# Kernel tuning notes

Hardware: AMD Instinct MI355X
Metric: run time of the kernel (lower is better)

The kernel has to match this reference:

```python
import jax, jax.numpy as jnp
import numpy as np

LN_EPS = 1e-5
NEG_SLOPE = 0.2
INF = float((1 << 32) - 1)


def _ln(x, g, b):
    m = x.mean(-1, keepdims=True)
    v = ((x - m) ** 2).mean(-1, keepdims=True)
    return (x - m) * jax.lax.rsqrt(v + LN_EPS) * g + b


def setup_inputs() -> dict:
    B, M, NPG = 128, 256, 192      # graphs, max nodes per graph, actual nodes per graph
    N = B * NPG                    # 24576 total nodes
    E = N * 16                     # 393216 edges (avg degree 16)
    d, H, Od = 256, 4, 64          # input/attn dim, heads, per-head dim
    out_dim = 256
    key = jax.random.key(0)
    ks = jax.random.split(key, 24)
    s = 0.05
    p = lambda k, sh: jax.random.normal(k, sh, jnp.float32) * s

    node_feat = jax.random.normal(ks[0], (N, d), jnp.float32)
    edge_feat = jax.random.normal(ks[1], (E, d), jnp.float32)
    edge_index = jax.random.randint(ks[2], (2, E), 0, N)
    ptr = jnp.arange(B + 1, dtype=jnp.int32) * NPG
    row_valid = jnp.arange(M) < NPG
    attn_mask = jnp.broadcast_to(row_valid[None, :, None] & row_valid[None, None, :], (B, M, M))

    return dict(
        node_feat=node_feat, attn_mask=attn_mask, edge_feat=edge_feat,
        edge_index=edge_index, num_nodes=N, ptr=ptr,
        Wq=p(ks[3], (d, H * Od)), Wk=p(ks[4], (d, H * Od)), Wv=p(ks[5], (d, H * Od)),
        alphaQ=p(ks[6], (H, Od)), alphaK=p(ks[7], (H, Od)), attn_bias=p(ks[8], (H, Od)),
        gin_eps=jnp.zeros((), jnp.float32),
        gin_W1=p(ks[9], (d, 2 * d)), gin_b1=jnp.zeros((2 * d,), jnp.float32),
        gin_W2=p(ks[10], (2 * d, d)), gin_b2=jnp.zeros((d,), jnp.float32),
        ln1_g=jnp.ones((d,), jnp.float32), ln1_b=jnp.zeros((d,), jnp.float32),
        ln2_g=jnp.ones((d,), jnp.float32), ln2_b=jnp.zeros((d,), jnp.float32),
        ff_W1=p(ks[11], (2 * d, out_dim)), ff_b1=jnp.zeros((out_dim,), jnp.float32),
        ff_W2=p(ks[12], (out_dim, out_dim)), ff_b2=jnp.zeros((out_dim,), jnp.float32),
    )


def reference(node_feat, attn_mask, edge_feat, edge_index, num_nodes, ptr,
              Wq, Wk, Wv, alphaQ, alphaK, attn_bias,
              gin_eps, gin_W1, gin_b1, gin_W2, gin_b2,
              ln1_g, ln1_b, ln2_g, ln2_b,
              ff_W1, ff_b1, ff_W2, ff_b2):
    B, M = attn_mask.shape[:2]
    N, d = node_feat.shape
    H = alphaQ.shape[0]

    # graph -> dense batch layout (scatter by (graph, local position))
    node_ids = jnp.arange(N)
    batch_id = jnp.searchsorted(ptr, node_ids, side='right') - 1
    local = node_ids - ptr[batch_id]
    attn_input = jnp.zeros((B, M, d), node_feat.dtype).at[batch_id, local].set(node_feat)

    # GAT-style additive multi-head attention
    Qp = (attn_input @ Wq).reshape(B, M, H, -1)
    Kp = (attn_input @ Wk).reshape(B, M, H, -1)
    Vp = (attn_input @ Wv).reshape(B, M, H, -1)
    aQ = jnp.einsum('bmhd,hd->bmh', Qp, alphaQ)
    aK = jnp.einsum('bmhd,hd->bmh', Kp, alphaK)
    w = jax.nn.leaky_relu(aQ[:, :, None, :] + aK[:, None, :, :], NEG_SLOPE)  # [B,Q,K,H]
    w = jnp.where(attn_mask[..., None], w, -INF)
    w = jax.nn.softmax(w, axis=2)
    attn_out = (jnp.einsum('bqkh,bkhd->bqhd', w, Vp) + attn_bias).reshape(B, M, -1)

    attn_res = _ln(attn_out + attn_input, ln1_g, ln1_b)[batch_id, local]  # back to [N, d]

    # GIN conv: relu(x[dst] + e) scatter-summed to src, then 2-layer MLP
    msg = jax.nn.relu(node_feat[edge_index[1]] + edge_feat)
    agg = jax.ops.segment_sum(msg, edge_index[0], num_segments=num_nodes)
    h = (1.0 + gin_eps) * node_feat + agg
    gin = jax.nn.relu(h @ gin_W1 + gin_b1) @ gin_W2 + gin_b2
    gin_res = _ln(gin + node_feat, ln2_g, ln2_b)

    x = jnp.concatenate([gin_res, attn_res], axis=-1)  # [N, 2d]
    return jax.nn.relu(x @ ff_W1 + ff_b1) @ ff_W2 + ff_b2
```

## Files before the change

### kernel.cpp

```cpp
#include <hip/hip_runtime.h>

#define LN_EPS 1e-5f
#define NEG_SLOPE 0.2f

typedef __attribute__((ext_vector_type(8))) short short8;
typedef __attribute__((ext_vector_type(4))) float f32x4;

__device__ __forceinline__ unsigned short f2bf(float f) {
  union { float f; unsigned int u; } v;
  v.f = f;
  unsigned int r = v.u + 0x7fffu + ((v.u >> 16) & 1u);
  return (unsigned short)(r >> 16);
}
__device__ __forceinline__ float bf2f(unsigned short u) {
  union { unsigned int u; float f; } v;
  v.u = ((unsigned int)u) << 16;
  return v.f;
}

__global__ __launch_bounds__(256) void k_fold(
    const float* __restrict__ Wq, const float* __restrict__ Wk,
    const float* __restrict__ alphaQ, const float* __restrict__ alphaK,
    float* __restrict__ wqa, float* __restrict__ wka) {
  int t = threadIdx.x;
  for (int h = 0; h < 4; ++h) {
    float sq = 0.f, sk = 0.f;
    for (int od = 0; od < 64; ++od) {
      sq += Wq[t * 256 + h * 64 + od] * alphaQ[h * 64 + od];
      sk += Wk[t * 256 + h * 64 + od] * alphaK[h * 64 + od];
    }
    wqa[t * 4 + h] = sq;
    wka[t * 4 + h] = sk;
  }
}

__global__ __launch_bounds__(256) void k_mega(
    const float* __restrict__ Wv, const float* __restrict__ gW1,
    const float* __restrict__ gW2, const float* __restrict__ fW1,
    const float* __restrict__ fW2, unsigned short* __restrict__ wvt,
    unsigned short* __restrict__ w1t, unsigned short* __restrict__ w2t,
    unsigned short* __restrict__ fw1t, unsigned short* __restrict__ fw2t,
    int* __restrict__ ideg, int Nn, const float* __restrict__ node_feat,
    unsigned short* __restrict__ nf16, const float* __restrict__ wqa,
    const float* __restrict__ wka, float* __restrict__ aQ,
    float* __restrict__ aK) {
  const int bid = blockIdx.x;
  if (bid < 2048) {
    int i = bid * 256 + threadIdx.x;
    const float* src;
    unsigned short* dst;
    int K, N, base;
    if (i < 65536) {
      src = Wv; dst = wvt; K = 256; N = 256; base = 0;
    } else if (i < 196608) {
      src = gW1; dst = w1t; K = 256; N = 512; base = 65536;
    } else if (i < 327680) {
      src = gW2; dst = w2t; K = 512; N = 256; base = 196608;
    } else if (i < 458752) {
      src = fW1; dst = fw1t; K = 512; N = 256; base = 327680;
    } else {
      src = fW2; dst = fw2t; K = 256; N = 256; base = 458752;
    }
    int j = i - base;
    int n = j / K, k = j - n * K;
    dst[j] = f2bf(src[(size_t)k * N + n]);
    return;
  }
  if (bid < 2144) {
    int i = (bid - 2048) * 256 + threadIdx.x;
    if (i < Nn) ideg[i] = 0;
    return;
  }
  const int n = (bid - 2144) * 4 + (threadIdx.x >> 6);
  const int lane = threadIdx.x & 63;
  f32x4 x = ((const f32x4*)node_feat)[(size_t)n * 64 + lane];
  ushort4 o;
  o.x = f2bf(x.x);
  o.y = f2bf(x.y);
  o.z = f2bf(x.z);
  o.w = f2bf(x.w);
  ((ushort4*)nf16)[(size_t)n * 64 + lane] = o;
  float sq[4], sk[4];
  const int d0 = lane * 4;
#pragma unroll
  for (int h = 0; h < 4; ++h) {
    sq[h] = x.x * wqa[(d0 + 0) * 4 + h] + x.y * wqa[(d0 + 1) * 4 + h] +
            x.z * wqa[(d0 + 2) * 4 + h] + x.w * wqa[(d0 + 3) * 4 + h];
    sk[h] = x.x * wka[(d0 + 0) * 4 + h] + x.y * wka[(d0 + 1) * 4 + h] +
            x.z * wka[(d0 + 2) * 4 + h] + x.w * wka[(d0 + 3) * 4 + h];
  }
#pragma unroll
  for (int off = 32; off; off >>= 1) {
#pragma unroll
    for (int h = 0; h < 4; ++h) {
      sq[h] += __shfl_xor(sq[h], off);
      sk[h] += __shfl_xor(sk[h], off);
    }
  }
  if (lane == 0) {
#pragma unroll
    for (int h = 0; h < 4; ++h) {
      aQ[(size_t)n * 4 + h] = sq[h];
      aK[(size_t)n * 4 + h] = sk[h];
    }
  }
}

template <bool RELU, bool BIAS, bool OUTBF>
__global__ __launch_bounds__(256) void k_gemm16(
    const unsigned short* __restrict__ A, const unsigned short* __restrict__ Bt,
    const float* __restrict__ bias, void* __restrict__ Cv, int M, int N,
    int K) {
  __shared__ uint4 As[512];
  __shared__ uint4 Bs[1024];
  const int tid = threadIdx.x;
  const int wid = tid >> 6;
  const int lane = tid & 63;
  const int row0 = blockIdx.x * 64;
  const int col0 = blockIdx.y * 128;
  const int wr = wid >> 1;
  const int wc = wid & 1;
  const int fr = lane & 15;
  const int fq = lane >> 4;

  f32x4 acc[2][4];
#pragma unroll
  for (int m = 0; m < 2; ++m)
#pragma unroll
    for (int n = 0; n < 4; ++n) acc[m][n] = (f32x4){0.f, 0.f, 0.f, 0.f};

  for (int k0 = 0; k0 < K; k0 += 64) {
    __syncthreads();
#pragma unroll
    for (int c = 0; c < 2; ++c) {
      int idx = c * 256 + tid;
      int row = idx >> 3, slot = idx & 7;
      As[row * 8 + (slot ^ (row & 7))] =
          *(const uint4*)(A + (size_t)(row0 + row) * K + k0 + slot * 8);
    }
#pragma unroll
    for (int c = 0; c < 4; ++c) {
      int idx = c * 256 + tid;
      int row = idx >> 3, slot = idx & 7;
      Bs[row * 8 + (slot ^ (row & 7))] =
          *(const uint4*)(Bt + (size_t)(col0 + row) * K + k0 + slot * 8);
    }
    __syncthreads();
#pragma unroll
    for (int kk = 0; kk < 2; ++kk) {
      short8 af[2], bfr[4];
#pragma unroll
      for (int m = 0; m < 2; ++m) {
        int row = wr * 32 + m * 16 + fr;
        af[m] = *(const short8*)&As[row * 8 + ((kk * 4 + fq) ^ (row & 7))];
      }
#pragma unroll
      for (int n = 0; n < 4; ++n) {
        int col = wc * 64 + n * 16 + fr;
        bfr[n] = *(const short8*)&Bs[col * 8 + ((kk * 4 + fq) ^ (col & 7))];
      }
#pragma unroll
      for (int m = 0; m < 2; ++m)
#pragma unroll
        for (int n = 0; n < 4; ++n)
          acc[m][n] = __builtin_amdgcn_mfma_f32_16x16x32_bf16(af[m], bfr[n],
                                                              acc[m][n], 0, 0, 0);
    }
  }

#pragma unroll
  for (int n = 0; n < 4; ++n) {
    const int col = col0 + wc * 64 + n * 16 + fr;
    const float bv = BIAS ? bias[col] : 0.f;
#pragma unroll
    for (int m = 0; m < 2; ++m) {
#pragma unroll
      for (int r = 0; r < 4; ++r) {
        int row = row0 + wr * 32 + m * 16 + fq * 4 + r;
        float v = acc[m][n][r];
        if (BIAS) v += bv;
        if (RELU) v = fmaxf(v, 0.f);
        if (OUTBF)
          ((unsigned short*)Cv)[(size_t)row * N + col] = f2bf(v);
        else
          ((float*)Cv)[(size_t)row * N + col] = v;
      }
    }
  }
}

__global__ __launch_bounds__(256) void k_attn(
    const float* __restrict__ aQ, const float* __restrict__ aK,
    const unsigned short* __restrict__ Vp16,
    const float* __restrict__ attn_bias, const int* __restrict__ ptr,
    unsigned short* __restrict__ attn16) {
  __shared__ unsigned short Vt[64 * 192];
  __shared__ float aQs[192], aKs[192], sinv[192];
  __shared__ float kmax_s;
  const int b = blockIdx.x, h = blockIdx.y;
  const int n0 = ptr[b];
  const int tid = threadIdx.x;
  const int wid = tid >> 6, lane = tid & 63;

  if (tid < 192) {
    aQs[tid] = aQ[(size_t)(n0 + tid) * 4 + h];
    aKs[tid] = aK[(size_t)(n0 + tid) * 4 + h];
  }
  for (int i = tid; i < 1536; i += 256) {
    int k = i >> 3, cc = (i & 7) << 3;
    short8 v = *(const short8*)(Vp16 + (size_t)(n0 + k) * 256 + h * 64 + cc);
    int ks = k >> 3, kr = k & 7;
#pragma unroll
    for (int jj = 0; jj < 8; ++jj) {
      int c = cc + jj;
      Vt[c * 192 + ((ks ^ (c & 7)) << 3) + kr] = (unsigned short)v[jj];
    }
  }
  __syncthreads();
  if (wid == 0) {
    float m3 = fmaxf(fmaxf(aKs[lane], aKs[lane + 64]), aKs[lane + 128]);
#pragma unroll
    for (int off = 32; off; off >>= 1) m3 = fmaxf(m3, __shfl_xor(m3, off));
    if (lane == 0) kmax_s = m3;
  }
  __syncthreads();
  const float kmax = kmax_s;
  const int fr = lane & 15, fq = lane >> 4;
  const int qbase = wid * 48;

  float aq_m[3], mm[3];
#pragma unroll
  for (int m = 0; m < 3; ++m) {
    float aqv = aQs[qbase + m * 16 + fr];
    aq_m[m] = aqv;
    float t = aqv + kmax;
    mm[m] = t > 0.f ? t : NEG_SLOPE * t;
  }

  f32x4 acc[3][4];
#pragma unroll
  for (int m = 0; m < 3; ++m)
#pragma unroll
    for (int n = 0; n < 4; ++n) acc[m][n] = (f32x4){0.f, 0.f, 0.f, 0.f};
  float psum[3] = {0.f, 0.f, 0.f};

  for (int ks = 0; ks < 6; ++ks) {
    short8 bf[4];
#pragma unroll
    for (int n = 0; n < 4; ++n) {
      int c = n * 16 + fr;
      bf[n] = *(const short8*)&Vt[c * 192 + ((((ks << 2) + fq) ^ (c & 7)) << 3)];
    }
    float ak[8];
#pragma unroll
    for (int j = 0; j < 8; ++j) ak[j] = aKs[(ks << 5) + (fq << 3) + j];
#pragma unroll
    for (int m = 0; m < 3; ++m) {
      short8 af;
      float ps = 0.f;
#pragma unroll
      for (int j = 0; j < 8; ++j) {
        float x = aq_m[m] + ak[j];
        x = x > 0.f ? x : NEG_SLOPE * x;
        float p = __expf(x - mm[m]);
        ps += p;
        af[j] = (short)f2bf(p);
      }
      psum[m] += ps;
#pragma unroll
      for (int n = 0; n < 4; ++n)
        acc[m][n] =
            __builtin_amdgcn_mfma_f32_16x16x32_bf16(af, bf[n], acc[m][n], 0, 0, 0);
    }
  }

#pragma unroll
  for (int m = 0; m < 3; ++m) {
    psum[m] += __shfl_xor(psum[m], 16);
    psum[m] += __shfl_xor(psum[m], 32);
  }
  if (fq == 0) {
#pragma unroll
    for (int m = 0; m < 3; ++m) sinv[qbase + m * 16 + fr] = 1.f / psum[m];
  }
  __syncthreads();

#pragma unroll
  for (int m = 0; m < 3; ++m) {
#pragma unroll
    for (int n = 0; n < 4; ++n) {
      int col = n * 16 + fr;
      float bv = attn_bias[h * 64 + col];
#pragma unroll
      for (int r = 0; r < 4; ++r) {
        int q = qbase + m * 16 + fq * 4 + r;
        float v = acc[m][n][r] * sinv[q] + bv;
        attn16[(size_t)(n0 + q) * 256 + h * 64 + col] = f2bf(v);
      }
    }
  }
}

template <bool XBF>
__global__ __launch_bounds__(64) void k_ln(
    const void* __restrict__ xin, const float* __restrict__ res,
    const float* __restrict__ g, const float* __restrict__ bt,
    unsigned short* __restrict__ out, int ostride, int ooff) {
  const int n = blockIdx.x;
  const int lane = threadIdx.x;
  float v0, v1, v2, v3;
  if (XBF) {
    ushort4 xv = *(const ushort4*)((const unsigned short*)xin +
                                   (size_t)n * 256 + lane * 4);
    v0 = bf2f(xv.x);
    v1 = bf2f(xv.y);
    v2 = bf2f(xv.z);
    v3 = bf2f(xv.w);
  } else {
    float4 xv = *(const float4*)((const float*)xin + (size_t)n * 256 + lane * 4);
    v0 = xv.x;
    v1 = xv.y;
    v2 = xv.z;
    v3 = xv.w;
  }
  float4 rv = *(const float4*)(res + (size_t)n * 256 + lane * 4);
  v0 += rv.x;
  v1 += rv.y;
  v2 += rv.z;
  v3 += rv.w;
  float s = v0 + v1 + v2 + v3;
  float ss = v0 * v0 + v1 * v1 + v2 * v2 + v3 * v3;
#pragma unroll
  for (int off = 32; off; off >>= 1) {
    s += __shfl_xor(s, off);
    ss += __shfl_xor(ss, off);
  }
  const float mean = s * (1.f / 256.f);
  const float var = ss * (1.f / 256.f) - mean * mean;
  const float rs = rsqrtf(var + LN_EPS);
  float4 gv = *(const float4*)(g + lane * 4);
  float4 bv = *(const float4*)(bt + lane * 4);
  ushort4 o;
  o.x = f2bf((v0 - mean) * rs * gv.x + bv.x);
  o.y = f2bf((v1 - mean) * rs * gv.y + bv.y);
  o.z = f2bf((v2 - mean) * rs * gv.z + bv.z);
  o.w = f2bf((v3 - mean) * rs * gv.w + bv.w);
  *(ushort4*)(out + (size_t)n * ostride + ooff + lane * 4) = o;
}

__global__ __launch_bounds__(256) void k_deg(const int* __restrict__ ei,
                                             int* __restrict__ deg, int E) {
  int e = blockIdx.x * 256 + threadIdx.x;
  if (e < E) atomicAdd(&deg[ei[e]], 1);
}

__global__ __launch_bounds__(1024) void k_scan(const int* __restrict__ deg,
                                               int* __restrict__ ofs,
                                               int* __restrict__ cursor,
                                               int Nn) {
  __shared__ int part[1024];
  const int t = threadIdx.x;
  const int CH = (Nn + 1023) / 1024;
  const int base = t * CH;
  int s = 0;
  for (int i = 0; i < CH; ++i) s += (base + i < Nn) ? deg[base + i] : 0;
  part[t] = s;
  __syncthreads();
  for (int off = 1; off < 1024; off <<= 1) {
    int v = (t >= off) ? part[t - off] : 0;
    __syncthreads();
    part[t] += v;
    __syncthreads();
  }
  int o = (t == 0) ? 0 : part[t - 1];
  for (int i = 0; i < CH; ++i) {
    if (base + i < Nn) {
      ofs[base + i] = o;
      cursor[base + i] = o;
      o += deg[base + i];
    }
  }
  if (t == 1023) ofs[Nn] = part[1023];
}

__global__ __launch_bounds__(256) void k_scatter(const int* __restrict__ ei,
                                                 int* __restrict__ cursor,
                                                 int2* __restrict__ edges,
                                                 int E) {
  int e = blockIdx.x * 256 + threadIdx.x;
  if (e < E) {
    int src = ei[e];
    int dst = ei[E + e];
    int pos = atomicAdd(&cursor[src], 1);
    edges[pos] = make_int2(e, dst);
  }
}

__global__ __launch_bounds__(64) void k_gather(
    const float* __restrict__ node, const float* __restrict__ ef,
    const int2* __restrict__ edges, const int* __restrict__ ofs,
    const float* __restrict__ eps_p, unsigned short* __restrict__ agg16) {
  const int n = blockIdx.x;
  const int lane = threadIdx.x;
  const int s0 = ofs[n];
  const int s1 = ofs[n + 1];
  const float epl = 1.f + eps_p[0];
  const f32x4* nodev = (const f32x4*)node;
  const f32x4* efv = (const f32x4*)ef;
  f32x4 xv = nodev[(size_t)n * 64 + lane];
  float a0 = epl * xv.x, a1 = epl * xv.y, a2 = epl * xv.z, a3 = epl * xv.w;
  int j = s0;
  for (; j + 4 <= s1; j += 4) {
    int2 ed0 = edges[j], ed1 = edges[j + 1], ed2 = edges[j + 2],
         ed3 = edges[j + 3];
    f32x4 e0 = __builtin_nontemporal_load(&efv[(size_t)ed0.x * 64 + lane]);
    f32x4 e1 = __builtin_nontemporal_load(&efv[(size_t)ed1.x * 64 + lane]);
    f32x4 e2 = __builtin_nontemporal_load(&efv[(size_t)ed2.x * 64 + lane]);
    f32x4 e3 = __builtin_nontemporal_load(&efv[(size_t)ed3.x * 64 + lane]);
    f32x4 m0 = nodev[(size_t)ed0.y * 64 + lane];
    f32x4 m1 = nodev[(size_t)ed1.y * 64 + lane];
    f32x4 m2 = nodev[(size_t)ed2.y * 64 + lane];
    f32x4 m3 = nodev[(size_t)ed3.y * 64 + lane];
    a0 += fmaxf(e0.x + m0.x, 0.f) + fmaxf(e1.x + m1.x, 0.f) +
          fmaxf(e2.x + m2.x, 0.f) + fmaxf(e3.x + m3.x, 0.f);
    a1 += fmaxf(e0.y + m0.y, 0.f) + fmaxf(e1.y + m1.y, 0.f) +
          fmaxf(e2.y + m2.y, 0.f) + fmaxf(e3.y + m3.y, 0.f);
    a2 += fmaxf(e0.z + m0.z, 0.f) + fmaxf(e1.z + m1.z, 0.f) +
          fmaxf(e2.z + m2.z, 0.f) + fmaxf(e3.z + m3.z, 0.f);
    a3 += fmaxf(e0.w + m0.w, 0.f) + fmaxf(e1.w + m1.w, 0.f) +
          fmaxf(e2.w + m2.w, 0.f) + fmaxf(e3.w + m3.w, 0.f);
  }
  for (; j < s1; ++j) {
    int2 ed = edges[j];
    f32x4 ev = __builtin_nontemporal_load(&efv[(size_t)ed.x * 64 + lane]);
    f32x4 mv = nodev[(size_t)ed.y * 64 + lane];
    a0 += fmaxf(ev.x + mv.x, 0.f);
    a1 += fmaxf(ev.y + mv.y, 0.f);
    a2 += fmaxf(ev.z + mv.z, 0.f);
    a3 += fmaxf(ev.w + mv.w, 0.f);
  }
  ushort4 o;
  o.x = f2bf(a0);
  o.y = f2bf(a1);
  o.z = f2bf(a2);
  o.w = f2bf(a3);
  *(ushort4*)(agg16 + (size_t)n * 256 + lane * 4) = o;
}

extern "C" void kernel_launch(void* const* d_in, const int* in_sizes, int n_in,
                              void* d_out, int out_size, void* d_ws,
                              size_t ws_size, hipStream_t stream) {
  const float* node_feat = (const float*)d_in[0];
  const float* edge_feat = (const float*)d_in[2];
  const int* edge_index = (const int*)d_in[3];
  const int* ptr = (const int*)d_in[5];
  const float* Wq = (const float*)d_in[6];
  const float* Wk = (const float*)d_in[7];
  const float* Wv = (const float*)d_in[8];
  const float* alphaQ = (const float*)d_in[9];
  const float* alphaK = (const float*)d_in[10];
  const float* attn_bias = (const float*)d_in[11];
  const float* gin_eps = (const float*)d_in[12];
  const float* gin_W1 = (const float*)d_in[13];
  const float* gin_b1 = (const float*)d_in[14];
  const float* gin_W2 = (const float*)d_in[15];
  const float* gin_b2 = (const float*)d_in[16];
  const float* ln1_g = (const float*)d_in[17];
  const float* ln1_b = (const float*)d_in[18];
  const float* ln2_g = (const float*)d_in[19];
  const float* ln2_b = (const float*)d_in[20];
  const float* ff_W1 = (const float*)d_in[21];
  const float* ff_b1 = (const float*)d_in[22];
  const float* ff_W2 = (const float*)d_in[23];
  const float* ff_b2 = (const float*)d_in[24];

  const int N = in_sizes[0] / 256;
  const int E = in_sizes[2] / 256;
  const int B = in_sizes[5] - 1;

  float* ws = (float*)d_ws;
  float* buf0 = ws;
  unsigned short* x2_16 = (unsigned short*)(buf0 + (size_t)N * 256);
  unsigned short* agg16 = x2_16 + (size_t)N * 512;
  unsigned short* t1_16 = agg16 + (size_t)N * 256;
  unsigned short* h1_16 = t1_16 + (size_t)N * 512;
  unsigned short* nf16 = h1_16 + (size_t)N * 256;
  unsigned short* vp16 = nf16 + (size_t)N * 256;
  unsigned short* at16 = vp16 + (size_t)N * 256;
  unsigned short* wvt = at16 + (size_t)N * 256;
  unsigned short* w1t = wvt + 65536;
  unsigned short* w2t = w1t + 131072;
  unsigned short* ffw1t = w2t + 131072;
  unsigned short* ffw2t = ffw1t + 131072;
  float* wqa = (float*)(ffw2t + 65536);
  float* wka = wqa + 1024;
  float* aQ = wka + 1024;
  float* aK = aQ + (size_t)N * 4;
  int* ideg = (int*)(aK + (size_t)N * 4);
  int* ofs = ideg + N;
  int* cursor = ofs + N + 2;
  int2* edges = (int2*)(cursor + N);
  size_t need = (size_t)N * 256 * 4 + (size_t)N * 2304 * 2 + 1100000 +
                (size_t)N * 8 * 4 + (size_t)N * 16 + (size_t)E * 8 + 8192;
  if (ws_size < need) return;

  k_fold<<<1, 256, 0, stream>>>(Wq, Wk, alphaQ, alphaK, wqa, wka);
  k_mega<<<2144 + N / 4, 256, 0, stream>>>(
      Wv, gin_W1, gin_W2, ff_W1, ff_W2, wvt, w1t, w2t, ffw1t, ffw2t, ideg, N,
      node_feat, nf16, wqa, wka, aQ, aK);

  k_gemm16<false, false, true><<<dim3(N / 64, 2), 256, 0, stream>>>(
      nf16, wvt, nullptr, vp16, N, 256, 256);
  k_attn<<<dim3(B, 4), 256, 0, stream>>>(aQ, aK, vp16, attn_bias, ptr, at16);
  k_ln<true><<<N, 64, 0, stream>>>(at16, node_feat, ln1_g, ln1_b, x2_16, 512,
                                   256);

  k_deg<<<(E + 255) / 256, 256, 0, stream>>>(edge_index, ideg, E);
  k_scan<<<1, 1024, 0, stream>>>(ideg, ofs, cursor, N);
  k_scatter<<<(E + 255) / 256, 256, 0, stream>>>(edge_index, cursor, edges, E);
  k_gather<<<N, 64, 0, stream>>>(node_feat, edge_feat, edges, ofs, gin_eps,
                                 agg16);
  k_gemm16<true, true, true><<<dim3(N / 64, 4), 256, 0, stream>>>(
      agg16, w1t, gin_b1, t1_16, N, 512, 256);
  k_gemm16<false, true, false><<<dim3(N / 64, 2), 256, 0, stream>>>(
      t1_16, w2t, gin_b2, buf0, N, 256, 512);
  k_ln<false><<<N, 64, 0, stream>>>(buf0, node_feat, ln2_g, ln2_b, x2_16, 512,
                                    0);

  k_gemm16<true, true, true><<<dim3(N / 64, 2), 256, 0, stream>>>(
      x2_16, ffw1t, ff_b1, h1_16, N, 256, 512);
  k_gemm16<false, true, false><<<dim3(N / 64, 2), 256, 0, stream>>>(
      h1_16, ffw2t, ff_b2, (float*)d_out, N, 256, 256);
}
```

Baseline: 343.7 us.

## Merge independent attention and GIN stages into combined role-dispatch kernels

Converts the GEMM, gather, attention and LN1 kernels into device role functions. Independent work is then packed into shared launches: V-projection GEMM with the GIN gather, attention with the GIN first GEMM, and GIN second GEMM with LN1. Degree counting moves into the mega prep kernel and ideg zeroing moves into k_fold. The goal is fewer launches and more concurrency between the two branches. The cost is uneven block roles within a launch, and shared-memory size is set by the largest role.

```diff
diff --git a/kernel.cpp b/kernel.cpp
--- a/kernel.cpp
+++ b/kernel.cpp
@@ -18,110 +18,20 @@
   return v.f;
 }
 
-__global__ __launch_bounds__(256) void k_fold(
-    const float* __restrict__ Wq, const float* __restrict__ Wk,
-    const float* __restrict__ alphaQ, const float* __restrict__ alphaK,
-    float* __restrict__ wqa, float* __restrict__ wka) {
-  int t = threadIdx.x;
-  for (int h = 0; h < 4; ++h) {
-    float sq = 0.f, sk = 0.f;
-    for (int od = 0; od < 64; ++od) {
-      sq += Wq[t * 256 + h * 64 + od] * alphaQ[h * 64 + od];
-      sk += Wk[t * 256 + h * 64 + od] * alphaK[h * 64 + od];
-    }
-    wqa[t * 4 + h] = sq;
-    wka[t * 4 + h] = sk;
-  }
-}
-
-__global__ __launch_bounds__(256) void k_mega(
-    const float* __restrict__ Wv, const float* __restrict__ gW1,
-    const float* __restrict__ gW2, const float* __restrict__ fW1,
-    const float* __restrict__ fW2, unsigned short* __restrict__ wvt,
-    unsigned short* __restrict__ w1t, unsigned short* __restrict__ w2t,
-    unsigned short* __restrict__ fw1t, unsigned short* __restrict__ fw2t,
-    int* __restrict__ ideg, int Nn, const float* __restrict__ node_feat,
-    unsigned short* __restrict__ nf16, const float* __restrict__ wqa,
-    const float* __restrict__ wka, float* __restrict__ aQ,
-    float* __restrict__ aK) {
-  const int bid = blockIdx.x;
-  if (bid < 2048) {
-    int i = bid * 256 + threadIdx.x;
-    const float* src;
-    unsigned short* dst;
-    int K, N, base;
-    if (i < 65536) {
-      src = Wv; dst = wvt; K = 256; N = 256; base = 0;
-    } else if (i < 196608) {
-      src = gW1; dst = w1t; K = 256; N = 512; base = 65536;
-    } else if (i < 327680) {
-      src = gW2; dst = w2t; K = 512; N = 256; base = 196608;
-    } else if (i < 458752) {
-      src = fW1; dst = fw1t; K = 512; N = 256; base = 327680;
-    } else {
-      src = fW2; dst = fw2t; K = 256; N = 256; base = 458752;
-    }
-    int j = i - base;
-    int n = j / K, k = j - n * K;
-    dst[j] = f2bf(src[(size_t)k * N + n]);
-    return;
-  }
-  if (bid < 2144) {
-    int i = (bid - 2048) * 256 + threadIdx.x;
-    if (i < Nn) ideg[i] = 0;
-    return;
-  }
-  const int n = (bid - 2144) * 4 + (threadIdx.x >> 6);
-  const int lane = threadIdx.x & 63;
-  f32x4 x = ((const f32x4*)node_feat)[(size_t)n * 64 + lane];
-  ushort4 o;
-  o.x = f2bf(x.x);
-  o.y = f2bf(x.y);
-  o.z = f2bf(x.z);
-  o.w = f2bf(x.w);
-  ((ushort4*)nf16)[(size_t)n * 64 + lane] = o;
-  float sq[4], sk[4];
-  const int d0 = lane * 4;
-#pragma unroll
-  for (int h = 0; h < 4; ++h) {
-    sq[h] = x.x * wqa[(d0 + 0) * 4 + h] + x.y * wqa[(d0 + 1) * 4 + h] +
-            x.z * wqa[(d0 + 2) * 4 + h] + x.w * wqa[(d0 + 3) * 4 + h];
-    sk[h] = x.x * wka[(d0 + 0) * 4 + h] + x.y * wka[(d0 + 1) * 4 + h] +
-            x.z * wka[(d0 + 2) * 4 + h] + x.w * wka[(d0 + 3) * 4 + h];
-  }
-#pragma unroll
-  for (int off = 32; off; off >>= 1) {
-#pragma unroll
-    for (int h = 0; h < 4; ++h) {
-      sq[h] += __shfl_xor(sq[h], off);
-      sk[h] += __shfl_xor(sk[h], off);
-    }
-  }
-  if (lane == 0) {
-#pragma unroll
-    for (int h = 0; h < 4; ++h) {
-      aQ[(size_t)n * 4 + h] = sq[h];
-      aK[(size_t)n * 4 + h] = sk[h];
-    }
-  }
-}
-
 template <bool RELU, bool BIAS, bool OUTBF>
-__global__ __launch_bounds__(256) void k_gemm16(
-    const unsigned short* __restrict__ A, const unsigned short* __restrict__ Bt,
-    const float* __restrict__ bias, void* __restrict__ Cv, int M, int N,
-    int K) {
-  __shared__ uint4 As[512];
-  __shared__ uint4 Bs[1024];
+__device__ __forceinline__ void gemm_role(
+    int t, char* smemc, const unsigned short* __restrict__ A,
+    const unsigned short* __restrict__ Bt, const float* __restrict__ bias,
+    void* __restrict__ Cv, int N, int K) {
+  uint4* As = (uint4*)smemc;
+  uint4* Bs = (uint4*)smemc + 512;
   const int tid = threadIdx.x;
-  const int wid = tid >> 6;
-  const int lane = tid & 63;
-  const int row0 = blockIdx.x * 64;
-  const int col0 = blockIdx.y * 128;
-  const int wr = wid >> 1;
-  const int wc = wid & 1;
-  const int fr = lane & 15;
-  const int fq = lane >> 4;
+  const int wid = tid >> 6, lane = tid & 63;
+  const int nC = N >> 7;
+  const int row0 = (t / nC) << 6;
+  const int col0 = (t % nC) << 7;
+  const int wr = wid >> 1, wc = wid & 1;
+  const int fr = lane & 15, fq = lane >> 4;
 
   f32x4 acc[2][4];
 #pragma unroll
@@ -189,219 +99,12 @@
   }
 }
 
-__global__ __launch_bounds__(256) void k_attn(
-    const float* __restrict__ aQ, const float* __restrict__ aK,
-    const unsigned short* __restrict__ Vp16,
-    const float* __restrict__ attn_bias, const int* __restrict__ ptr,
-    unsigned short* __restrict__ attn16) {
-  __shared__ unsigned short Vt[64 * 192];
-  __shared__ float aQs[192], aKs[192], sinv[192];
-  __shared__ float kmax_s;
-  const int b = blockIdx.x, h = blockIdx.y;
-  const int n0 = ptr[b];
-  const int tid = threadIdx.x;
-  const int wid = tid >> 6, lane = tid & 63;
-
-  if (tid < 192) {
-    aQs[tid] = aQ[(size_t)(n0 + tid) * 4 + h];
-    aKs[tid] = aK[(size_t)(n0 + tid) * 4 + h];
-  }
-  for (int i = tid; i < 1536; i += 256) {
-    int k = i >> 3, cc = (i & 7) << 3;
-    short8 v = *(const short8*)(Vp16 + (size_t)(n0 + k) * 256 + h * 64 + cc);
-    int ks = k >> 3, kr = k & 7;
-#pragma unroll
-    for (int jj = 0; jj < 8; ++jj) {
-      int c = cc + jj;
-      Vt[c * 192 + ((ks ^ (c & 7)) << 3) + kr] = (unsigned short)v[jj];
-    }
-  }
-  __syncthreads();
-  if (wid == 0) {
-    float m3 = fmaxf(fmaxf(aKs[lane], aKs[lane + 64]), aKs[lane + 128]);
-#pragma unroll
-    for (int off = 32; off; off >>= 1) m3 = fmaxf(m3, __shfl_xor(m3, off));
-    if (lane == 0) kmax_s = m3;
-  }
-  __syncthreads();
-  const float kmax = kmax_s;
-  const int fr = lane & 15, fq = lane >> 4;
-  const int qbase = wid * 48;
-
-  float aq_m[3], mm[3];
-#pragma unroll
-  for (int m = 0; m < 3; ++m) {
-    float aqv = aQs[qbase + m * 16 + fr];
-    aq_m[m] = aqv;
-    float t = aqv + kmax;
-    mm[m] = t > 0.f ? t : NEG_SLOPE * t;
-  }
-
-  f32x4 acc[3][4];
-#pragma unroll
-  for (int m = 0; m < 3; ++m)
-#pragma unroll
-    for (int n = 0; n < 4; ++n) acc[m][n] = (f32x4){0.f, 0.f, 0.f, 0.f};
-  float psum[3] = {0.f, 0.f, 0.f};
-
-  for (int ks = 0; ks < 6; ++ks) {
-    short8 bf[4];
-#pragma unroll
-    for (int n = 0; n < 4; ++n) {
-      int c = n * 16 + fr;
-      bf[n] = *(const short8*)&Vt[c * 192 + ((((ks << 2) + fq) ^ (c & 7)) << 3)];
-    }
-    float ak[8];
-#pragma unroll
-    for (int j = 0; j < 8; ++j) ak[j] = aKs[(ks << 5) + (fq << 3) + j];
-#pragma unroll
-    for (int m = 0; m < 3; ++m) {
-      short8 af;
-      float ps = 0.f;
-#pragma unroll
-      for (int j = 0; j < 8; ++j) {
-        float x = aq_m[m] + ak[j];
-        x = x > 0.f ? x : NEG_SLOPE * x;
-        float p = __expf(x - mm[m]);
-        ps += p;
-        af[j] = (short)f2bf(p);
-      }
-      psum[m] += ps;
-#pragma unroll
-      for (int n = 0; n < 4; ++n)
-        acc[m][n] =
-            __builtin_amdgcn_mfma_f32_16x16x32_bf16(af, bf[n], acc[m][n], 0, 0, 0);
-    }
-  }
-
-#pragma unroll
-  for (int m = 0; m < 3; ++m) {
-    psum[m] += __shfl_xor(psum[m], 16);
-    psum[m] += __shfl_xor(psum[m], 32);
-  }
-  if (fq == 0) {
-#pragma unroll
-    for (int m = 0; m < 3; ++m) sinv[qbase + m * 16 + fr] = 1.f / psum[m];
-  }
-  __syncthreads();
-
-#pragma unroll
-  for (int m = 0; m < 3; ++m) {
-#pragma unroll
-    for (int n = 0; n < 4; ++n) {
-      int col = n * 16 + fr;
-      float bv = attn_bias[h * 64 + col];
-#pragma unroll
-      for (int r = 0; r < 4; ++r) {
-        int q = qbase + m * 16 + fq * 4 + r;
-        float v = acc[m][n][r] * sinv[q] + bv;
-        attn16[(size_t)(n0 + q) * 256 + h * 64 + col] = f2bf(v);
-      }
-    }
-  }
-}
-
-template <bool XBF>
-__global__ __launch_bounds__(64) void k_ln(
-    const void* __restrict__ xin, const float* __restrict__ res,
-    const float* __restrict__ g, const float* __restrict__ bt,
-    unsigned short* __restrict__ out, int ostride, int ooff) {
-  const int n = blockIdx.x;
-  const int lane = threadIdx.x;
-  float v0, v1, v2, v3;
-  if (XBF) {
-    ushort4 xv = *(const ushort4*)((const unsigned short*)xin +
-                                   (size_t)n * 256 + lane * 4);
-    v0 = bf2f(xv.x);
-    v1 = bf2f(xv.y);
-    v2 = bf2f(xv.z);
-    v3 = bf2f(xv.w);
-  } else {
-    float4 xv = *(const float4*)((const float*)xin + (size_t)n * 256 + lane * 4);
-    v0 = xv.x;
-    v1 = xv.y;
-    v2 = xv.z;
-    v3 = xv.w;
-  }
-  float4 rv = *(const float4*)(res + (size_t)n * 256 + lane * 4);
-  v0 += rv.x;
-  v1 += rv.y;
-  v2 += rv.z;
-  v3 += rv.w;
-  float s = v0 + v1 + v2 + v3;
-  float ss = v0 * v0 + v1 * v1 + v2 * v2 + v3 * v3;
-#pragma unroll
-  for (int off = 32; off; off >>= 1) {
-    s += __shfl_xor(s, off);
-    ss += __shfl_xor(ss, off);
-  }
-  const float mean = s * (1.f / 256.f);
-  const float var = ss * (1.f / 256.f) - mean * mean;
-  const float rs = rsqrtf(var + LN_EPS);
-  float4 gv = *(const float4*)(g + lane * 4);
-  float4 bv = *(const float4*)(bt + lane * 4);
-  ushort4 o;
-  o.x = f2bf((v0 - mean) * rs * gv.x + bv.x);
-  o.y = f2bf((v1 - mean) * rs * gv.y + bv.y);
-  o.z = f2bf((v2 - mean) * rs * gv.z + bv.z);
-  o.w = f2bf((v3 - mean) * rs * gv.w + bv.w);
-  *(ushort4*)(out + (size_t)n * ostride + ooff + lane * 4) = o;
-}
-
-__global__ __launch_bounds__(256) void k_deg(const int* __restrict__ ei,
-                                             int* __restrict__ deg, int E) {
-  int e = blockIdx.x * 256 + threadIdx.x;
-  if (e < E) atomicAdd(&deg[ei[e]], 1);
-}
-
-__global__ __launch_bounds__(1024) void k_scan(const int* __restrict__ deg,
-                                               int* __restrict__ ofs,
-                                               int* __restrict__ cursor,
-                                               int Nn) {
-  __shared__ int part[1024];
-  const int t = threadIdx.x;
-  const int CH = (Nn + 1023) / 1024;
-  const int base = t * CH;
-  int s = 0;
-  for (int i = 0; i < CH; ++i) s += (base + i < Nn) ? deg[base + i] : 0;
-  part[t] = s;
-  __syncthreads();
-  for (int off = 1; off < 1024; off <<= 1) {
-    int v = (t >= off) ? part[t - off] : 0;
-    __syncthreads();
-    part[t] += v;
-    __syncthreads();
-  }
-  int o = (t == 0) ? 0 : part[t - 1];
-  for (int i = 0; i < CH; ++i) {
-    if (base + i < Nn) {
-      ofs[base + i] = o;
-      cursor[base + i] = o;
-      o += deg[base + i];
-    }
-  }
-  if (t == 1023) ofs[Nn] = part[1023];
-}
-
-__global__ __launch_bounds__(256) void k_scatter(const int* __restrict__ ei,
-                                                 int* __restrict__ cursor,
-                                                 int2* __restrict__ edges,
-                                                 int E) {
-  int e = blockIdx.x * 256 + threadIdx.x;
-  if (e < E) {
-    int src = ei[e];
-    int dst = ei[E + e];
-    int pos = atomicAdd(&cursor[src], 1);
-    edges[pos] = make_int2(e, dst);
-  }
-}
-
-__global__ __launch_bounds__(64) void k_gather(
-    const float* __restrict__ node, const float* __restrict__ ef,
+__device__ __forceinline__ void gather_role(
+    int t, const float* __restrict__ node, const float* __restrict__ ef,
     const int2* __restrict__ edges, const int* __restrict__ ofs,
     const float* __restrict__ eps_p, unsigned short* __restrict__ agg16) {
-  const int n = blockIdx.x;
-  const int lane = threadIdx.x;
+  const int n = t * 4 + (threadIdx.x >> 6);
+  const int lane = threadIdx.x & 63;
   const int s0 = ofs[n];
   const int s1 = ofs[n + 1];
   const float epl = 1.f + eps_p[0];
@@ -447,6 +150,365 @@
   *(ushort4*)(agg16 + (size_t)n * 256 + lane * 4) = o;
 }
 
+__device__ __forceinline__ void attn_role(
+    int t, char* smemc, const float* __restrict__ aQ,
+    const float* __restrict__ aK, const unsigned short* __restrict__ Vp16,
+    const float* __restrict__ attn_bias, const int* __restrict__ ptr,
+    unsigned short* __restrict__ attn16) {
+  unsigned short* Vt = (unsigned short*)smemc;
+  float* aQs = (float*)(smemc + 24576);
+  float* aKs = aQs + 192;
+  float* sinv = aKs + 192;
+  float* kmax_s = sinv + 192;
+  const int b = t >> 2, h = t & 3;
+  const int n0 = ptr[b];
+  const int tid = threadIdx.x;
+  const int wid = tid >> 6, lane = tid & 63;
+
+  if (tid < 192) {
+    aQs[tid] = aQ[(size_t)(n0 + tid) * 4 + h];
+    aKs[tid] = aK[(size_t)(n0 + tid) * 4 + h];
+  }
+  for (int i = tid; i < 1536; i += 256) {
+    int k = i >> 3, cc = (i & 7) << 3;
+    short8 v = *(const short8*)(Vp16 + (size_t)(n0 + k) * 256 + h * 64 + cc);
+    int ks = k >> 3, kr = k & 7;
+#pragma unroll
+    for (int jj = 0; jj < 8; ++jj) {
+      int c = cc + jj;
+      Vt[c * 192 + ((ks ^ (c & 7)) << 3) + kr] = (unsigned short)v[jj];
+    }
+  }
+  __syncthreads();
+  if (wid == 0) {
+    float m3 = fmaxf(fmaxf(aKs[lane], aKs[lane + 64]), aKs[lane + 128]);
+#pragma unroll
+    for (int off = 32; off; off >>= 1) m3 = fmaxf(m3, __shfl_xor(m3, off));
+    if (lane == 0) kmax_s[0] = m3;
+  }
+  __syncthreads();
+  const float kmax = kmax_s[0];
+  const int fr = lane & 15, fq = lane >> 4;
+  const int qbase = wid * 48;
+
+  float aq_m[3], mm[3];
+#pragma unroll
+  for (int m = 0; m < 3; ++m) {
+    float aqv = aQs[qbase + m * 16 + fr];
+    aq_m[m] = aqv;
+    float tt = aqv + kmax;
+    mm[m] = tt > 0.f ? tt : NEG_SLOPE * tt;
+  }
+
+  f32x4 acc[3][4];
+#pragma unroll
+  for (int m = 0; m < 3; ++m)
+#pragma unroll
+    for (int n = 0; n < 4; ++n) acc[m][n] = (f32x4){0.f, 0.f, 0.f, 0.f};
+  float psum[3] = {0.f, 0.f, 0.f};
+
+  for (int ks = 0; ks < 6; ++ks) {
+    short8 bf[4];
+#pragma unroll
+    for (int n = 0; n < 4; ++n) {
+      int c = n * 16 + fr;
+      bf[n] = *(const short8*)&Vt[c * 192 + ((((ks << 2) + fq) ^ (c & 7)) << 3)];
+    }
+    float ak[8];
+#pragma unroll
+    for (int j = 0; j < 8; ++j) ak[j] = aKs[(ks << 5) + (fq << 3) + j];
+#pragma unroll
+    for (int m = 0; m < 3; ++m) {
+      short8 af;
+      float ps = 0.f;
+#pragma unroll
+      for (int j = 0; j < 8; ++j) {
+        float x = aq_m[m] + ak[j];
+        x = x > 0.f ? x : NEG_SLOPE * x;
+        float p = __expf(x - mm[m]);
+        ps += p;
+        af[j] = (short)f2bf(p);
+      }
+      psum[m] += ps;
+#pragma unroll
+      for (int n = 0; n < 4; ++n)
+        acc[m][n] =
+            __builtin_amdgcn_mfma_f32_16x16x32_bf16(af, bf[n], acc[m][n], 0, 0, 0);
+    }
+  }
+
+#pragma unroll
+  for (int m = 0; m < 3; ++m) {
+    psum[m] += __shfl_xor(psum[m], 16);
+    psum[m] += __shfl_xor(psum[m], 32);
+  }
+  if (fq == 0) {
+#pragma unroll
+    for (int m = 0; m < 3; ++m) sinv[qbase + m * 16 + fr] = 1.f / psum[m];
+  }
+  __syncthreads();
+
+#pragma unroll
+  for (int m = 0; m < 3; ++m) {
+#pragma unroll
+    for (int n = 0; n < 4; ++n) {
+      int col = n * 16 + fr;
+      float bv = attn_bias[h * 64 + col];
+#pragma unroll
+      for (int r = 0; r < 4; ++r) {
+        int q = qbase + m * 16 + fq * 4 + r;
+        float v = acc[m][n][r] * sinv[q] + bv;
+        attn16[(size_t)(n0 + q) * 256 + h * 64 + col] = f2bf(v);
+      }
+    }
+  }
+}
+
+__device__ __forceinline__ void ln1_role(
+    int t, const unsigned short* __restrict__ xin,
+    const float* __restrict__ res, const float* __restrict__ g,
+    const float* __restrict__ bt, unsigned short* __restrict__ out) {
+  const int n = t * 4 + (threadIdx.x >> 6);
+  const int lane = threadIdx.x & 63;
+  ushort4 xv = *(const ushort4*)(xin + (size_t)n * 256 + lane * 4);
+  float v0 = bf2f(xv.x), v1 = bf2f(xv.y), v2 = bf2f(xv.z), v3 = bf2f(xv.w);
+  float4 rv = *(const float4*)(res + (size_t)n * 256 + lane * 4);
+  v0 += rv.x;
+  v1 += rv.y;
+  v2 += rv.z;
+  v3 += rv.w;
+  float s = v0 + v1 + v2 + v3;
+  float ss = v0 * v0 + v1 * v1 + v2 * v2 + v3 * v3;
+#pragma unroll
+  for (int off = 32; off; off >>= 1) {
+    s += __shfl_xor(s, off);
+    ss += __shfl_xor(ss, off);
+  }
+  const float mean = s * (1.f / 256.f);
+  const float var = ss * (1.f / 256.f) - mean * mean;
+  const float rs = rsqrtf(var + LN_EPS);
+  float4 gv = *(const float4*)(g + lane * 4);
+  float4 bv = *(const float4*)(bt + lane * 4);
+  ushort4 o;
+  o.x = f2bf((v0 - mean) * rs * gv.x + bv.x);
+  o.y = f2bf((v1 - mean) * rs * gv.y + bv.y);
+  o.z = f2bf((v2 - mean) * rs * gv.z + bv.z);
+  o.w = f2bf((v3 - mean) * rs * gv.w + bv.w);
+  *(ushort4*)(out + (size_t)n * 512 + 256 + lane * 4) = o;
+}
+
+__global__ __launch_bounds__(256) void k_fold(
+    const float* __restrict__ Wq, const float* __restrict__ Wk,
+    const float* __restrict__ alphaQ, const float* __restrict__ alphaK,
+    float* __restrict__ wqa, float* __restrict__ wka, int* __restrict__ ideg,
+    int Nn) {
+  int t = threadIdx.x;
+  for (int i = t; i < Nn; i += 256) ideg[i] = 0;
+  for (int h = 0; h < 4; ++h) {
+    float sq = 0.f, sk = 0.f;
+    for (int od = 0; od < 64; ++od) {
+      sq += Wq[t * 256 + h * 64 + od] * alphaQ[h * 64 + od];
+      sk += Wk[t * 256 + h * 64 + od] * alphaK[h * 64 + od];
+    }
+    wqa[t * 4 + h] = sq;
+    wka[t * 4 + h] = sk;
+  }
+}
+
+__global__ __launch_bounds__(256) void k_mega(
+    const float* __restrict__ Wv, const float* __restrict__ gW1,
+    const float* __restrict__ gW2, const float* __restrict__ fW1,
+    const float* __restrict__ fW2, unsigned short* __restrict__ wvt,
+    unsigned short* __restrict__ w1t, unsigned short* __restrict__ w2t,
+    unsigned short* __restrict__ fw1t, unsigned short* __restrict__ fw2t,
+    const int* __restrict__ ei, int* __restrict__ ideg, int E,
+    const float* __restrict__ node_feat, unsigned short* __restrict__ nf16,
+    const float* __restrict__ wqa, const float* __restrict__ wka,
+    float* __restrict__ aQ, float* __restrict__ aK) {
+  const int bid = blockIdx.x;
+  if (bid < 2048) {
+    int i = bid * 256 + threadIdx.x;
+    const float* src;
+    unsigned short* dst;
+    int K, N, base;
+    if (i < 65536) {
+      src = Wv; dst = wvt; K = 256; N = 256; base = 0;
+    } else if (i < 196608) {
+      src = gW1; dst = w1t; K = 256; N = 512; base = 65536;
+    } else if (i < 327680) {
+      src = gW2; dst = w2t; K = 512; N = 256; base = 196608;
+    } else if (i < 458752) {
+      src = fW1; dst = fw1t; K = 512; N = 256; base = 327680;
+    } else {
+      src = fW2; dst = fw2t; K = 256; N = 256; base = 458752;
+    }
+    int j = i - base;
+    int n = j / K, k = j - n * K;
+    dst[j] = f2bf(src[(size_t)k * N + n]);
+    return;
+  }
+  if (bid < 3584) {
+    int e = (bid - 2048) * 256 + threadIdx.x;
+    if (e < E) atomicAdd(&ideg[ei[e]], 1);
+    return;
+  }
+  const int n = (bid - 3584) * 4 + (threadIdx.x >> 6);
+  const int lane = threadIdx.x & 63;
+  f32x4 x = ((const f32x4*)node_feat)[(size_t)n * 64 + lane];
+  ushort4 o;
+  o.x = f2bf(x.x);
+  o.y = f2bf(x.y);
+  o.z = f2bf(x.z);
+  o.w = f2bf(x.w);
+  ((ushort4*)nf16)[(size_t)n * 64 + lane] = o;
+  float sq[4], sk[4];
+  const int d0 = lane * 4;
+#pragma unroll
+  for (int h = 0; h < 4; ++h) {
+    sq[h] = x.x * wqa[(d0 + 0) * 4 + h] + x.y * wqa[(d0 + 1) * 4 + h] +
+            x.z * wqa[(d0 + 2) * 4 + h] + x.w * wqa[(d0 + 3) * 4 + h];
+    sk[h] = x.x * wka[(d0 + 0) * 4 + h] + x.y * wka[(d0 + 1) * 4 + h] +
+            x.z * wka[(d0 + 2) * 4 + h] + x.w * wka[(d0 + 3) * 4 + h];
+  }
+#pragma unroll
+  for (int off = 32; off; off >>= 1) {
+#pragma unroll
+    for (int h = 0; h < 4; ++h) {
+      sq[h] += __shfl_xor(sq[h], off);
+      sk[h] += __shfl_xor(sk[h], off);
+    }
+  }
+  if (lane == 0) {
+#pragma unroll
+    for (int h = 0; h < 4; ++h) {
+      aQ[(size_t)n * 4 + h] = sq[h];
+      aK[(size_t)n * 4 + h] = sk[h];
+    }
+  }
+}
+
+__global__ __launch_bounds__(1024) void k_scan(const int* __restrict__ deg,
+                                               int* __restrict__ ofs,
+                                               int* __restrict__ cursor,
+                                               int Nn) {
+  __shared__ int part[1024];
+  const int t = threadIdx.x;
+  const int CH = (Nn + 1023) / 1024;
+  const int base = t * CH;
+  int s = 0;
+  for (int i = 0; i < CH; ++i) s += (base + i < Nn) ? deg[base + i] : 0;
+  part[t] = s;
+  __syncthreads();
+  for (int off = 1; off < 1024; off <<= 1) {
+    int v = (t >= off) ? part[t - off] : 0;
+    __syncthreads();
+    part[t] += v;
+    __syncthreads();
+  }
+  int o = (t == 0) ? 0 : part[t - 1];
+  for (int i = 0; i < CH; ++i) {
+    if (base + i < Nn) {
+      ofs[base + i] = o;
+      cursor[base + i] = o;
+      o += deg[base + i];
+    }
+  }
+  if (t == 1023) ofs[Nn] = part[1023];
+}
+
+__global__ __launch_bounds__(256) void k_scatter(const int* __restrict__ ei,
+                                                 int* __restrict__ cursor,
+                                                 int2* __restrict__ edges,
+                                                 int E) {
+  int e = blockIdx.x * 256 + threadIdx.x;
+  if (e < E) {
+    int src = ei[e];
+    int dst = ei[E + e];
+    int pos = atomicAdd(&cursor[src], 1);
+    edges[pos] = make_int2(e, dst);
+  }
+}
+
+__global__ __launch_bounds__(256) void k_gv(
+    int nbV, const unsigned short* __restrict__ nf16,
+    const unsigned short* __restrict__ wvt, unsigned short* __restrict__ vp16,
+    const float* __restrict__ node, const float* __restrict__ ef,
+    const int2* __restrict__ edges, const int* __restrict__ ofs,
+    const float* __restrict__ eps_p, unsigned short* __restrict__ agg16) {
+  __shared__ __align__(16) char smem[24576];
+  if ((int)blockIdx.x < nbV)
+    gemm_role<false, false, true>(blockIdx.x, smem, nf16, wvt, nullptr, vp16,
+                                  256, 256);
+  else
+    gather_role(blockIdx.x - nbV, node, ef, edges, ofs, eps_p, agg16);
+}
+
+__global__ __launch_bounds__(256) void k_fa(
+    int nbA, const float* __restrict__ aQ, const float* __restrict__ aK,
+    const unsigned short* __restrict__ vp16,
+    const float* __restrict__ attn_bias, const int* __restrict__ ptr,
+    unsigned short* __restrict__ at16, const unsigned short* __restrict__ agg16,
+    const unsigned short* __restrict__ w1t, const float* __restrict__ gin_b1,
+    unsigned short* __restrict__ t1_16) {
+  __shared__ __align__(16) char smem[26944];
+  if ((int)blockIdx.x < nbA)
+    attn_role(blockIdx.x, smem, aQ, aK, vp16, attn_bias, ptr, at16);
+  else
+    gemm_role<true, true, true>(blockIdx.x - nbA, smem, agg16, w1t, gin_b1,
+                                t1_16, 512, 256);
+}
+
+__global__ __launch_bounds__(256) void k_f2l(
+    int nbG, const unsigned short* __restrict__ t1_16,
+    const unsigned short* __restrict__ w2t, const float* __restrict__ gin_b2,
+    float* __restrict__ buf0, const unsigned short* __restrict__ at16,
+    const float* __restrict__ node_feat, const float* __restrict__ g,
+    const float* __restrict__ bt, unsigned short* __restrict__ x2_16) {
+  __shared__ __align__(16) char smem[24576];
+  if ((int)blockIdx.x < nbG)
+    gemm_role<false, true, false>(blockIdx.x, smem, t1_16, w2t, gin_b2, buf0,
+                                  256, 512);
+  else
+    ln1_role(blockIdx.x - nbG, at16, node_feat, g, bt, x2_16);
+}
+
+template <bool RELU, bool BIAS, bool OUTBF>
+__global__ __launch_bounds__(256) void k_gemm(
+    const unsigned short* __restrict__ A, const unsigned short* __restrict__ Bt,
+    const float* __restrict__ bias, void* __restrict__ Cv, int N, int K) {
+  __shared__ __align__(16) char smem[24576];
+  gemm_role<RELU, BIAS, OUTBF>(blockIdx.x, smem, A, Bt, bias, Cv, N, K);
+}
+
+__global__ __launch_bounds__(64) void k_ln2(
+    const float* __restrict__ xin, const float* __restrict__ res,
+    const float* __restrict__ g, const float* __restrict__ bt,
+    unsigned short* __restrict__ out) {
+  const int n = blockIdx.x;
+  const int lane = threadIdx.x;
+  float4 xv = *(const float4*)(xin + (size_t)n * 256 + lane * 4);
+  float4 rv = *(const float4*)(res + (size_t)n * 256 + lane * 4);
+  float v0 = xv.x + rv.x, v1 = xv.y + rv.y, v2 = xv.z + rv.z, v3 = xv.w + rv.w;
+  float s = v0 + v1 + v2 + v3;
+  float ss = v0 * v0 + v1 * v1 + v2 * v2 + v3 * v3;
+#pragma unroll
+  for (int off = 32; off; off >>= 1) {
+    s += __shfl_xor(s, off);
+    ss += __shfl_xor(ss, off);
+  }
+  const float mean = s * (1.f / 256.f);
+  const float var = ss * (1.f / 256.f) - mean * mean;
+  const float rs = rsqrtf(var + LN_EPS);
+  float4 gv = *(const float4*)(g + lane * 4);
+  float4 bv = *(const float4*)(bt + lane * 4);
+  ushort4 o;
+  o.x = f2bf((v0 - mean) * rs * gv.x + bv.x);
+  o.y = f2bf((v1 - mean) * rs * gv.y + bv.y);
+  o.z = f2bf((v2 - mean) * rs * gv.z + bv.z);
+  o.w = f2bf((v3 - mean) * rs * gv.w + bv.w);
+  *(ushort4*)(out + (size_t)n * 512 + lane * 4) = o;
+}
+
 extern "C" void kernel_launch(void* const* d_in, const int* in_sizes, int n_in,
                               void* d_out, int out_size, void* d_ws,
                               size_t ws_size, hipStream_t stream) {
@@ -504,31 +566,33 @@
                 (size_t)N * 8 * 4 + (size_t)N * 16 + (size_t)E * 8 + 8192;
   if (ws_size < need) return;
 
-  k_fold<<<1, 256, 0, stream>>>(Wq, Wk, alphaQ, alphaK, wqa, wka);
-  k_mega<<<2144 + N / 4, 256, 0, stream>>>(
-      Wv, gin_W1, gin_W2, ff_W1, ff_W2, wvt, w1t, w2t, ffw1t, ffw2t, ideg, N,
-      node_feat, nf16, wqa, wka, aQ, aK);
-
-  k_gemm16<false, false, true><<<dim3(N / 64, 2), 256, 0, stream>>>(
-      nf16, wvt, nullptr, vp16, N, 256, 256);
-  k_attn<<<dim3(B, 4), 256, 0, stream>>>(aQ, aK, vp16, attn_bias, ptr, at16);
-  k_ln<true><<<N, 64, 0, stream>>>(at16, node_feat, ln1_g, ln1_b, x2_16, 512,
-                                   256);
-
-  k_deg<<<(E + 255) / 256, 256, 0, stream>>>(edge_index, ideg, E);
+  const int degB = (E + 255) / 256;
+
+  k_fold<<<1, 256, 0, stream>>>(Wq, Wk, alphaQ, alphaK, wqa, wka, ideg, N);
+  k_mega<<<2048 + degB + N / 4, 256, 0, stream>>>(
+      Wv, gin_W1, gin_W2, ff_W1, ff_W2, wvt, w1t, w2t, ffw1t, ffw2t,
+      edge_index, ideg, E, node_feat, nf16, wqa, wka, aQ, aK);
+
   k_scan<<<1, 1024, 0, stream>>>(ideg, ofs, cursor, N);
-  k_scatter<<<(E + 255) / 256, 256, 0, stream>>>(edge_index, cursor, edges, E);
-  k_gather<<<N, 64, 0, stream>>>(node_feat, edge_feat, edges, ofs, gin_eps,
-                                 agg16);
-  k_gemm16<true, true, true><<<dim3(N / 64, 4), 256, 0, stream>>>(
-      agg16, w1t, gin_b1, t1_16, N, 512, 256);
-  k_gemm16<false, true, false><<<dim3(N / 64, 2), 256, 0, stream>>>(
-      t1_16, w2t, gin_b2, buf0, N, 256, 512);
-  k_ln<false><<<N, 64, 0, stream>>>(buf0, node_feat, ln2_g, ln2_b, x2_16, 512,
-                                    0);
-
-  k_gemm16<true, true, true><<<dim3(N / 64, 2), 256, 0, stream>>>(
-      x2_16, ffw1t, ff_b1, h1_16, N, 256, 512);
-  k_gemm16<false, true, false><<<dim3(N / 64, 2), 256, 0, stream>>>(
-      h1_16, ffw2t, ff_b2, (float*)d_out, N, 256, 256);
-}
+  k_scatter<<<degB, 256, 0, stream>>>(edge_index, cursor, edges, E);
+
+  const int nbV = (N / 64) * 2;
+  k_gv<<<nbV + N / 4, 256, 0, stream>>>(nbV, nf16, wvt, vp16, node_feat,
+                                        edge_feat, edges, ofs, gin_eps, agg16);
+
+  const int nbA = B * 4;
+  k_fa<<<nbA + (N / 64) * 4, 256, 0, stream>>>(nbA, aQ, aK, vp16, attn_bias,
+                                               ptr, at16, agg16, w1t, gin_b1,
+                                               t1_16);
+
+  const int nbG = (N / 64) * 2;
+  k_f2l<<<nbG + N / 4, 256, 0, stream>>>(nbG, t1_16, w2t, gin_b2, buf0, at16,
+                                         node_feat, ln1_g, ln1_b, x2_16);
+
+  k_ln2<<<N, 64, 0, stream>>>(buf0, node_feat, ln2_g, ln2_b, x2_16);
+  k_gemm<true, true, true><<<(N / 64) * 2, 256, 0, stream>>>(x2_16, ffw1t,
+                                                             ff_b1, h1_16, 256,
+                                                             512);
+  k_gemm<false, true, false><<<(N / 64) * 2, 256, 0, stream>>>(
+      h1_16, ffw2t, ff_b2, d_out, 256, 256);
+}
```

Result: faster. 334.7 us (-2.6%).
